# Kernel tuning notes

Measured on AMD Instinct MI355X. Metric: run time of the kernel, lower is better.

The kernel has to match this reference:

```python
import jax, jax.numpy as jnp
import numpy as np

POOLING_COUNTS = [15, 8, 8, 8]
N = 128


def _build_entries():
    """Replicates SparseMaxPool.__init__: per step (kernel, pool_stride, i_idx, j_idx)."""
    entries = []
    stride, offset = 1, 0
    for ci, c in enumerate(POOLING_COUNTS):
        for k in range(c):
            offset += stride
            # pooler layout: first block all MaxPool1d(2,1); later blocks start with MaxPool1d(3,2)
            kernel = 3 if (ci > 0 and k == 0) else 2
            pstride = 2 if kernel == 3 else 1
            i = np.arange(0, N - offset, stride)
            j = np.arange(offset, N, stride)
            entries.append((kernel, pstride, i, j))
        stride *= 2
    return entries

_ENTRIES = _build_entries()


def _maxpool1d(x, kernel, stride):
    # x: [B, D, L] -> [B, D, (L-kernel)//stride + 1]
    L = x.shape[-1]
    out = (L - kernel) // stride + 1
    slices = [x[..., t : t + (out - 1) * stride + 1 : stride] for t in range(kernel)]
    y = slices[0]
    for s in slices[1:]:
        y = jnp.maximum(y, s)
    return y


def setup_inputs() -> dict:
    key = jax.random.key(0)
    x = jax.random.normal(key, (16, 256, N), dtype=jnp.float32)
    return {"x": x}


def reference(x):
    B, D, Nv = x.shape
    map2d = jnp.zeros((B, D, N, N), dtype=x.dtype)
    diag = np.arange(N)
    map2d = map2d.at[:, :, diag, diag].set(x)
    for kernel, pstride, i, j in _ENTRIES:
        x = _maxpool1d(x, kernel, pstride)
        map2d = map2d.at[:, :, i, j].set(x)
    return map2d
```

## Files before the change

kernel.cpp:

```cpp
#include <hip/hip_runtime.h>


#define NN 128
#define SLICE_ELEMS (NN * NN)

__device__ __forceinline__ void win_params(int o, int& lb, int& d2) {
    int w = o + 1;
    int k = 31 - __clz(w);
    int p2 = 1 << k;
    lb = 129 * k - (p2 - 1);
    d2 = w - p2;
}

__global__ __launch_bounds__(256) void sparse_maxpool_kernel(
        const float* __restrict__ x, float* __restrict__ out) {
    __shared__ float buf[784];
    const int tid = threadIdx.x;
    const int slice = blockIdx.x;
    float* __restrict__ out_s = out + (size_t)slice * SLICE_ELEMS;

    if (tid < NN) buf[tid] = x[(size_t)slice * NN + tid];

    float4 z = make_float4(0.f, 0.f, 0.f, 0.f);
    float4* __restrict__ o4 = reinterpret_cast<float4*>(out_s);
    #pragma unroll
    for (int it = 0; it < 16; ++it)
        o4[it * 256 + tid] = z;

    __syncthreads();
    int base_prev = 0, base_cur = NN;
    #pragma unroll
    for (int k = 1; k <= 7; ++k) {
        int half = 1 << (k - 1);
        int len = (NN + 1) - (1 << k);
        if (tid < len)
            buf[base_cur + tid] = fmaxf(buf[base_prev + tid], buf[base_prev + tid + half]);
        __syncthreads();
        base_prev = base_cur;
        base_cur += len;
    }

    {
        int o = tid & 15, lb, d2;
        win_params(o, lb, d2);
        int r0 = tid >> 4;
        #pragma unroll
        for (int jj = 0; jj < 8; ++jj) {
            int r = r0 + 16 * jj;
            if (r + o < NN)
                out_s[r * 129 + o] = fmaxf(buf[lb + r], buf[lb + r + d2]);
        }
    }
    {
        int o = 17 + 2 * (tid & 7), lb, d2;
        win_params(o, lb, d2);
        int r0 = 2 * (tid >> 3);
        #pragma unroll
        for (int jj = 0; jj < 2; ++jj) {
            int r = r0 + 64 * jj;
            if (r + o < NN)
                out_s[r * 129 + o] = fmaxf(buf[lb + r], buf[lb + r + d2]);
        }
    }
    {
        int o = 35 + 4 * (tid & 7), lb, d2;
        win_params(o, lb, d2);
        int r = 4 * (tid >> 3);
        if (r + o < NN)
            out_s[r * 129 + o] = fmaxf(buf[lb + r], buf[lb + r + d2]);
    }
    {
        int o = 71 + 8 * (tid & 7), lb, d2;
        win_params(o, lb, d2);
        int r = 8 * (tid >> 3);
        if (r + o < NN)
            out_s[r * 129 + o] = fmaxf(buf[lb + r], buf[lb + r + d2]);
    }
}

extern "C" void kernel_launch(void* const* d_in, const int* in_sizes, int n_in,
                              void* d_out, int out_size, void* d_ws, size_t ws_size,
                              hipStream_t stream) {
    const float* x = (const float*)d_in[0];
    float* out = (float*)d_out;
    const int slices = in_sizes[0] / NN;
    sparse_maxpool_kernel<<<dim3(slices), dim3(256), 0, stream>>>(x, out);
}
```

Measured before the change: 260.1 us.

## Build each output slice in LDS tile, stream out with nontemporal stores, persistent blocks

The kernel now assembles each 128x128 output slice in a 64KB shared-memory tile and writes it to global memory as full float4 nontemporal stores. Previously it issued a zero-fill pass followed by scattered scalar diagonal writes. Each block handles 8 slices in a grid-stride loop, and the tile is zeroed only once because the same sparse positions get overwritten for every slice. This removes the double write and the uncoalesced scatter to HBM. In exchange, the 64KB of LDS per block limits occupancy, and the grid shrinks to 512 blocks.

```diff
diff --git a/kernel.cpp b/kernel.cpp
--- a/kernel.cpp
+++ b/kernel.cpp
@@ -3,6 +3,8 @@
 
 #define NN 128
 #define SLICE_ELEMS (NN * NN)
+
+typedef float f32x4 __attribute__((ext_vector_type(4)));
 
 __device__ __forceinline__ void win_params(int o, int& lb, int& d2) {
     int w = o + 1;
@@ -13,68 +15,89 @@
 }
 
 __global__ __launch_bounds__(256) void sparse_maxpool_kernel(
-        const float* __restrict__ x, float* __restrict__ out) {
+        const float* __restrict__ x, float* __restrict__ out,
+        int n_slices, int spb) {
+    __shared__ float tile[SLICE_ELEMS];
     __shared__ float buf[784];
     const int tid = threadIdx.x;
-    const int slice = blockIdx.x;
-    float* __restrict__ out_s = out + (size_t)slice * SLICE_ELEMS;
 
-    if (tid < NN) buf[tid] = x[(size_t)slice * NN + tid];
-
-    float4 z = make_float4(0.f, 0.f, 0.f, 0.f);
-    float4* __restrict__ o4 = reinterpret_cast<float4*>(out_s);
+    f32x4 z = (f32x4)0.f;
+    f32x4* __restrict__ t4 = reinterpret_cast<f32x4*>(tile);
     #pragma unroll
     for (int it = 0; it < 16; ++it)
-        o4[it * 256 + tid] = z;
+        t4[it * 256 + tid] = z;
 
+    int slice = blockIdx.x;
+    if (slice < n_slices && tid < NN)
+        buf[tid] = x[(size_t)slice * NN + tid];
     __syncthreads();
-    int base_prev = 0, base_cur = NN;
-    #pragma unroll
-    for (int k = 1; k <= 7; ++k) {
-        int half = 1 << (k - 1);
-        int len = (NN + 1) - (1 << k);
-        if (tid < len)
-            buf[base_cur + tid] = fmaxf(buf[base_prev + tid], buf[base_prev + tid + half]);
+
+    for (int s = 0; s < spb; ++s, slice += gridDim.x) {
+        int base_prev = 0, base_cur = NN;
+        #pragma unroll
+        for (int k = 1; k <= 7; ++k) {
+            int half = 1 << (k - 1);
+            int len = (NN + 1) - (1 << k);
+            if (tid < len)
+                buf[base_cur + tid] = fmaxf(buf[base_prev + tid], buf[base_prev + tid + half]);
+            __syncthreads();
+            base_prev = base_cur;
+            base_cur += len;
+        }
+
+        if (slice < n_slices) {
+            {
+                int o = tid & 15, lb, d2;
+                win_params(o, lb, d2);
+                int r0 = tid >> 4;
+                #pragma unroll
+                for (int jj = 0; jj < 8; ++jj) {
+                    int r = r0 + 16 * jj;
+                    if (r + o < NN)
+                        tile[r * 129 + o] = fmaxf(buf[lb + r], buf[lb + r + d2]);
+                }
+            }
+            {
+                int o = 17 + 2 * (tid & 7), lb, d2;
+                win_params(o, lb, d2);
+                int r0 = 2 * (tid >> 3);
+                #pragma unroll
+                for (int jj = 0; jj < 2; ++jj) {
+                    int r = r0 + 64 * jj;
+                    if (r + o < NN)
+                        tile[r * 129 + o] = fmaxf(buf[lb + r], buf[lb + r + d2]);
+                }
+            }
+            {
+                int o = 35 + 4 * (tid & 7), lb, d2;
+                win_params(o, lb, d2);
+                int r = 4 * (tid >> 3);
+                if (r + o < NN)
+                    tile[r * 129 + o] = fmaxf(buf[lb + r], buf[lb + r + d2]);
+            }
+            {
+                int o = 71 + 8 * (tid & 7), lb, d2;
+                win_params(o, lb, d2);
+                int r = 8 * (tid >> 3);
+                if (r + o < NN)
+                    tile[r * 129 + o] = fmaxf(buf[lb + r], buf[lb + r + d2]);
+            }
+        }
         __syncthreads();
-        base_prev = base_cur;
-        base_cur += len;
-    }
 
-    {
-        int o = tid & 15, lb, d2;
-        win_params(o, lb, d2);
-        int r0 = tid >> 4;
-        #pragma unroll
-        for (int jj = 0; jj < 8; ++jj) {
-            int r = r0 + 16 * jj;
-            if (r + o < NN)
-                out_s[r * 129 + o] = fmaxf(buf[lb + r], buf[lb + r + d2]);
+        int nslice = slice + gridDim.x;
+        if (slice < n_slices) {
+            f32x4* __restrict__ o4 =
+                reinterpret_cast<f32x4*>(out + (size_t)slice * SLICE_ELEMS);
+            #pragma unroll
+            for (int it = 0; it < 16; ++it) {
+                int idx = it * 256 + tid;
+                __builtin_nontemporal_store(t4[idx], &o4[idx]);
+            }
         }
-    }
-    {
-        int o = 17 + 2 * (tid & 7), lb, d2;
-        win_params(o, lb, d2);
-        int r0 = 2 * (tid >> 3);
-        #pragma unroll
-        for (int jj = 0; jj < 2; ++jj) {
-            int r = r0 + 64 * jj;
-            if (r + o < NN)
-                out_s[r * 129 + o] = fmaxf(buf[lb + r], buf[lb + r + d2]);
-        }
-    }
-    {
-        int o = 35 + 4 * (tid & 7), lb, d2;
-        win_params(o, lb, d2);
-        int r = 4 * (tid >> 3);
-        if (r + o < NN)
-            out_s[r * 129 + o] = fmaxf(buf[lb + r], buf[lb + r + d2]);
-    }
-    {
-        int o = 71 + 8 * (tid & 7), lb, d2;
-        win_params(o, lb, d2);
-        int r = 8 * (tid >> 3);
-        if (r + o < NN)
-            out_s[r * 129 + o] = fmaxf(buf[lb + r], buf[lb + r + d2]);
+        if (nslice < n_slices && tid < NN)
+            buf[tid] = x[(size_t)nslice * NN + tid];
+        __syncthreads();
     }
 }
 
@@ -84,5 +107,7 @@
     const float* x = (const float*)d_in[0];
     float* out = (float*)d_out;
     const int slices = in_sizes[0] / NN;
-    sparse_maxpool_kernel<<<dim3(slices), dim3(256), 0, stream>>>(x, out);
+    const int spb = 8;
+    int nb = (slices + spb - 1) / spb;
+    sparse_maxpool_kernel<<<dim3(nb), dim3(256), 0, stream>>>(x, out, slices, spb);
 }
```

Result: slower. 270.7 us (+4.1%).
